# Kernel optimization log

Measured on AMD Instinct MI355X. Metric: run time of the kernel, lower is better.

The kernel has to match this reference:

```python
import jax, jax.numpy as jnp
import numpy as np

HIDDEN = 256
GROUPS = 4
GDIM = HIDDEN // GROUPS  # 64


def setup_inputs() -> dict:
    key = jax.random.key(0)
    k1, k2, k3, k4 = jax.random.split(key, 4)
    B, N, P = 8, 300, 32
    x = jax.random.normal(k1, (B, N, P, HIDDEN), dtype=jnp.float32)
    query_content = jax.random.normal(k2, (B, N, HIDDEN), dtype=jnp.float32)
    out_dim = GDIM * GDIM * GROUPS
    # nn.Linear default init: U(-1/sqrt(fan_in), 1/sqrt(fan_in))
    bound = 1.0 / np.sqrt(HIDDEN)
    W_gen = jax.random.uniform(k3, (HIDDEN, out_dim), dtype=jnp.float32, minval=-bound, maxval=bound)
    b_gen = jax.random.uniform(k4, (out_dim,), dtype=jnp.float32, minval=-bound, maxval=bound)
    gamma = jnp.ones((HIDDEN,), dtype=jnp.float32)
    beta = jnp.zeros((HIDDEN,), dtype=jnp.float32)
    return {"x": x, "query_content": query_content, "W_gen": W_gen, "b_gen": b_gen, "gamma": gamma, "beta": beta}


def _layer_norm(h, gamma, beta, eps=1e-5):
    mu = jnp.mean(h, axis=-1, keepdims=True)
    var = jnp.var(h, axis=-1, keepdims=True)
    return (h - mu) * jax.lax.rsqrt(var + eps) * gamma + beta


def reference(x, query_content, W_gen, b_gen, gamma, beta):
    B, N, P, C = x.shape
    # dynamic per-query weights: [B,N,G,gd,gd]
    w = (query_content @ W_gen + b_gen).reshape(B, N, GROUPS, GDIM, GDIM)
    xg = x.reshape(B, N, P, GROUPS, GDIM)
    # mixed[...,p,g,e] = sum_d xg[...,p,g,d] * w[...,g,e,d]  (matmul with W^T)
    mixed = jnp.einsum('bnpgd,bnged->bnpge', xg, w).reshape(B, N, P, C)
    return jax.nn.relu(_layer_norm(mixed, gamma, beta))
```

## Files before the change

kernel.cpp:

```cpp
#include <hip/hip_runtime.h>
#include <hip/hip_bf16.h>

typedef __attribute__((ext_vector_type(4))) float floatx4;
typedef __attribute__((ext_vector_type(8))) short short8;

#define HIDDEN 256
#define NOUT 16384

static __device__ __forceinline__ short bf16bits(float x) {
    __hip_bfloat16 h = __float2bfloat16(x);
    return __builtin_bit_cast(short, h);
}

#define GLDS16(gsrc, ldst) \
    __builtin_amdgcn_global_load_lds((const __attribute__((address_space(1))) void*)(gsrc), \
                                     (__attribute__((address_space(3))) void*)(ldst), 16, 0, 0)

static __device__ __forceinline__ int permc(int c) {
    const int g = c >> 12, e = (c >> 6) & 63, d = c & 63;
    const int nt = e >> 4, lq = e & 15, ks = (d >> 5) & 1, quad = (d >> 3) & 3, j = d & 7;
    return ((((g << 2) | nt) << 1 | ks) << 9) | (((quad << 4) | lq) << 3) | j;
}
static __device__ __forceinline__ int invperm(int p) {
    const int blk = p >> 9, g = blk >> 3, nt = (blk >> 1) & 3, ks = blk & 1;
    const int r = (p >> 3) & 63, quad = r >> 4, lq = r & 15, j = p & 7;
    return g * 4096 + (nt * 16 + lq) * 64 + ks * 32 + quad * 8 + j;
}

__global__ __launch_bounds__(256) void kPrep(
    const float* __restrict__ Wg, short* __restrict__ WgTp,
    const float* __restrict__ qc, short* __restrict__ qcb, int n4)
{
    __shared__ short t[64 * 68];
    const int tid = threadIdx.x;

    if (blockIdx.x < 1024) {
        const int n0 = (blockIdx.x & 255) * 64, k0 = (blockIdx.x >> 8) * 64;
        const int r  = tid >> 4;
        const int c4 = tid & 15;
        #pragma unroll
        for (int i = 0; i < 4; ++i) {
            const int kl = r + i * 16;
            float4 f = *reinterpret_cast<const float4*>(Wg + (size_t)(k0 + kl) * NOUT + n0 + c4 * 4);
            short4 v;
            v.x = bf16bits(f.x); v.y = bf16bits(f.y); v.z = bf16bits(f.z); v.w = bf16bits(f.w);
            *reinterpret_cast<short4*>(&t[kl * 68 + c4 * 4]) = v;
        }
        __syncthreads();
        #pragma unroll
        for (int h = 0; h < 2; ++h) {
            const int id = tid + h * 256;
            const int nl = id >> 3, kc = id & 7;
            short8 v;
            #pragma unroll
            for (int j = 0; j < 8; ++j) v[j] = t[(kc * 8 + j) * 68 + nl];
            const int prow = permc(n0 + nl);
            *reinterpret_cast<short8*>(WgTp + (size_t)prow * HIDDEN + k0 + kc * 8) = v;
        }
    } else {
        const int i = (blockIdx.x - 1024) * 256 + tid;
        if (i < n4) {
            float4 f = reinterpret_cast<const float4*>(qc)[i];
            short4 v;
            v.x = bf16bits(f.x); v.y = bf16bits(f.y); v.z = bf16bits(f.z); v.w = bf16bits(f.w);
            reinterpret_cast<short4*>(qcb)[i] = v;
        }
    }
}

__global__ __launch_bounds__(256) void kA5(
    const short* __restrict__ qcb, const short* __restrict__ WgTp,
    const float* __restrict__ bg, short* __restrict__ wdyn, int M)
{
    __shared__ short As[128 * 64];
    __shared__ short Bs[128 * 64];

    const int tid  = threadIdx.x;
    const int wave = tid >> 6, lane = tid & 63;
    const int lq   = lane & 15, quad = lane >> 4;
    const int wm   = wave >> 1, wn = wave & 1;
    const int m0   = blockIdx.x * 128;
    const int n0   = blockIdx.y * 128;

    const short* aSrc[4]; const short* bSrc[4];
    short* aDst[4]; short* bDst[4];
    #pragma unroll
    for (int t = 0; t < 4; ++t) {
        const int chunk = t * 256 + wave * 64 + lane;
        const int row = chunk >> 3, kc = chunk & 7;
        const int kcs = kc ^ (row & 7);
        int rA = m0 + row; if (rA >= M) rA = M - 1;
        aSrc[t] = qcb  + (size_t)rA * HIDDEN + kcs * 8;
        bSrc[t] = WgTp + (size_t)(n0 + row) * HIDDEN + kcs * 8;
        aDst[t] = &As[(t * 256 + wave * 64) * 8];
        bDst[t] = &Bs[(t * 256 + wave * 64) * 8];
    }

    int aOff[2][4], bOff[2][4];
    #pragma unroll
    for (int ks = 0; ks < 2; ++ks)
        #pragma unroll
        for (int i = 0; i < 4; ++i) {
            const int ra = wm * 64 + i * 16 + lq;
            aOff[ks][i] = ra * 64 + (((ks * 4 + quad) ^ (ra & 7)) * 8);
            const int rb = wn * 64 + i * 16 + lq;
            bOff[ks][i] = rb * 64 + (((ks * 4 + quad) ^ (rb & 7)) * 8);
        }

    floatx4 acc[4][4];
    #pragma unroll
    for (int i = 0; i < 4; ++i)
        #pragma unroll
        for (int j = 0; j < 4; ++j) acc[i][j] = (floatx4){0.f, 0.f, 0.f, 0.f};

    for (int it = 0; it < 4; ++it) {
        #pragma unroll
        for (int t = 0; t < 4; ++t) {
            GLDS16(aSrc[t], aDst[t]);
            GLDS16(bSrc[t], bDst[t]);
            aSrc[t] += 64; bSrc[t] += 64;
        }
        __syncthreads();

        #pragma unroll
        for (int ks = 0; ks < 2; ++ks) {
            short8 a[4], b[4];
            #pragma unroll
            for (int i = 0; i < 4; ++i) a[i] = *reinterpret_cast<const short8*>(&As[aOff[ks][i]]);
            #pragma unroll
            for (int j = 0; j < 4; ++j) b[j] = *reinterpret_cast<const short8*>(&Bs[bOff[ks][j]]);
            #pragma unroll
            for (int i = 0; i < 4; ++i)
                #pragma unroll
                for (int j = 0; j < 4; ++j)
                    acc[i][j] = __builtin_amdgcn_mfma_f32_16x16x32_bf16(a[i], b[j], acc[i][j], 0, 0, 0);
        }
        __syncthreads();
    }

    float bv[4];
    #pragma unroll
    for (int j = 0; j < 4; ++j) bv[j] = bg[invperm(n0 + wn * 64 + j * 16 + lq)];

    short* Cs = As;
    #pragma unroll
    for (int half = 0; half < 2; ++half) {
        if (half) __syncthreads();
        if (wm == half) {
            #pragma unroll
            for (int j = 0; j < 4; ++j)
                #pragma unroll
                for (int i = 0; i < 4; ++i)
                    #pragma unroll
                    for (int r = 0; r < 4; ++r)
                        Cs[(i * 16 + quad * 4 + r) * 128 + wn * 64 + j * 16 + lq] =
                            bf16bits(acc[i][j][r] + bv[j]);
        }
        __syncthreads();
        #pragma unroll
        for (int t = 0; t < 4; ++t) {
            const int id = t * 256 + tid;
            const int mr = id >> 4, ch = id & 15;
            const int grow = m0 + half * 64 + mr;
            if (grow < M)
                *reinterpret_cast<short8*>(&wdyn[(size_t)grow * NOUT + n0 + ch * 8]) =
                    *reinterpret_cast<const short8*>(&Cs[mr * 128 + ch * 8]);
        }
    }
}

__global__ __launch_bounds__(256) void kB6(
    const float* __restrict__ x, const short* __restrict__ wdyn,
    const float* __restrict__ gamma, const float* __restrict__ beta,
    float* __restrict__ out)
{
    __shared__ float ots[16 * 256];
    __shared__ float red[2][2][16][2];

    const int tid  = threadIdx.x;
    const int bnq  = blockIdx.x;
    const int wave = tid >> 6, lane = tid & 63;
    const int lq   = lane & 15, quad = lane >> 4;
    const int mtile = wave & 1, gp = wave >> 1;

    const float* xr = x + (size_t)bnq * (32 * HIDDEN) + (mtile * 16 + lq) * HIDDEN;
    const short* wr = wdyn + (size_t)bnq * NOUT + lane * 8;

    floatx4 xf[2][2][2];
    #pragma unroll
    for (int gi = 0; gi < 2; ++gi) {
        const int g = gp * 2 + gi;
        #pragma unroll
        for (int ks = 0; ks < 2; ++ks) {
            const floatx4* s = reinterpret_cast<const floatx4*>(xr + g * 64 + ks * 32 + quad * 8);
            xf[gi][ks][0] = __builtin_nontemporal_load(s);
            xf[gi][ks][1] = __builtin_nontemporal_load(s + 1);
        }
    }
    short8 afr[2][2];
    #pragma unroll
    for (int gi = 0; gi < 2; ++gi)
        #pragma unroll
        for (int ks = 0; ks < 2; ++ks) {
            const floatx4 f0 = xf[gi][ks][0];
            const floatx4 f1 = xf[gi][ks][1];
            short8 v;
            v[0]=bf16bits(f0[0]); v[1]=bf16bits(f0[1]); v[2]=bf16bits(f0[2]); v[3]=bf16bits(f0[3]);
            v[4]=bf16bits(f1[0]); v[5]=bf16bits(f1[1]); v[6]=bf16bits(f1[2]); v[7]=bf16bits(f1[3]);
            afr[gi][ks] = v;
        }

    floatx4 acc[2][4];
    #pragma unroll
    for (int gi = 0; gi < 2; ++gi)
        #pragma unroll
        for (int nt = 0; nt < 4; ++nt) acc[gi][nt] = (floatx4){0.f, 0.f, 0.f, 0.f};

    #pragma unroll
    for (int gi = 0; gi < 2; ++gi) {
        const int g = gp * 2 + gi;
        #pragma unroll
        for (int ks = 0; ks < 2; ++ks) {
            short8 b[4];
            #pragma unroll
            for (int nt = 0; nt < 4; ++nt)
                b[nt] = *reinterpret_cast<const short8*>(
                    wr + (((((g << 2) | nt) << 1) | ks) << 9));
            #pragma unroll
            for (int nt = 0; nt < 4; ++nt)
                acc[gi][nt] = __builtin_amdgcn_mfma_f32_16x16x32_bf16(
                    b[nt], afr[gi][ks], acc[gi][nt], 0, 0, 0);
        }
    }

    float s = 0.f, ss = 0.f;
    #pragma unroll
    for (int gi = 0; gi < 2; ++gi)
        #pragma unroll
        for (int nt = 0; nt < 4; ++nt)
            #pragma unroll
            for (int r = 0; r < 4; ++r) {
                const float v = acc[gi][nt][r];
                s += v; ss += v * v;
            }
    s  += __shfl_xor(s, 16);  ss += __shfl_xor(ss, 16);
    s  += __shfl_xor(s, 32);  ss += __shfl_xor(ss, 32);

    if (quad == 0) { red[mtile][gp][lq][0] = s; red[mtile][gp][lq][1] = ss; }
    __syncthreads();

    const float S  = s  + red[mtile][gp ^ 1][lq][0];
    const float SS = ss + red[mtile][gp ^ 1][lq][1];
    const float mu = S * (1.f / 256.f);
    float var = SS * (1.f / 256.f) - mu * mu;
    var = fmaxf(var, 0.f);
    const float rs = rsqrtf(var + 1e-5f);

    #pragma unroll
    for (int gi = 0; gi < 2; ++gi) {
        const int g = gp * 2 + gi;
        #pragma unroll
        for (int nt = 0; nt < 4; ++nt) {
            const int c0 = g * 64 + nt * 16 + quad * 4;
            const floatx4 gm = *reinterpret_cast<const floatx4*>(gamma + c0);
            const floatx4 bt = *reinterpret_cast<const floatx4*>(beta + c0);
            #pragma unroll
            for (int r = 0; r < 4; ++r)
                acc[gi][nt][r] = fmaxf((acc[gi][nt][r] - mu) * rs * gm[r] + bt[r], 0.f);
        }
    }

    floatx4* ots4 = reinterpret_cast<floatx4*>(ots);
    floatx4* obase = reinterpret_cast<floatx4*>(out + (size_t)bnq * (32 * HIDDEN));
    #pragma unroll
    for (int h = 0; h < 2; ++h) {
        if (h) __syncthreads();
        if (mtile == h) {
            #pragma unroll
            for (int gi = 0; gi < 2; ++gi) {
                const int g = gp * 2 + gi;
                #pragma unroll
                for (int nt = 0; nt < 4; ++nt) {
                    const int c4 = g * 16 + nt * 4 + quad;
                    ots4[(lq * 64 + c4) ^ (lq & 7)] = acc[gi][nt];
                }
            }
        }
        __syncthreads();
        #pragma unroll
        for (int t = 0; t < 4; ++t) {
            const int sl = t * 256 + tid;
            const int pl = sl >> 6;
            const floatx4 v = ots4[sl ^ (pl & 7)];
            __builtin_nontemporal_store(v, obase + h * 1024 + sl);
        }
    }
}

extern "C" void kernel_launch(void* const* d_in, const int* in_sizes, int n_in,
                              void* d_out, int out_size, void* d_ws, size_t ws_size,
                              hipStream_t stream)
{
    const float* x     = (const float*)d_in[0];
    const float* qc    = (const float*)d_in[1];
    const float* Wg    = (const float*)d_in[2];
    const float* bg    = (const float*)d_in[3];
    const float* gamma = (const float*)d_in[4];
    const float* beta  = (const float*)d_in[5];
    float* out = (float*)d_out;

    const int M = in_sizes[1] / HIDDEN;

    char* ws = (char*)d_ws;
    short* wdyn = (short*)ws;
    short* WgTp = (short*)(ws + (size_t)M * NOUT * 2);
    short* qcb  = (short*)(ws + (size_t)M * NOUT * 2 + (size_t)NOUT * HIDDEN * 2);

    const int n4 = (M * HIDDEN) / 4;
    const int prepBlocks = 1024 + (n4 + 255) / 256;
    kPrep<<<prepBlocks, 256, 0, stream>>>(Wg, WgTp, qc, qcb, n4);

    kA5<<<dim3((M + 127) / 128, NOUT / 128), 256, 0, stream>>>(qcb, WgTp, bg, wdyn, M);

    kB6<<<M, 256, 0, stream>>>(x, wdyn, gamma, beta, out);
}
```

Before: 217.3 us.

## Pre-swizzle GEMM operands into MFMA fragment order and load directly to registers

The prep kernel now writes the bf16 weight and query matrices in a fragment-tiled layout that matches the 16x16x32 MFMA operand layout. The GEMM then reads each operand straight from global memory into registers with double-buffered prefetch, dropping the LDS staging and barriers. Work-group indices are also remapped so each XCD handles a contiguous band of N tiles, which should improve L2 reuse of the weight panel. In exchange, operand tiles are re-read from global/L2 by each wave without LDS sharing, and M rows past the last 16-row tile are clamped to tile 0, which assumes M is a multiple of 16.

```diff
diff --git a/kernel.cpp b/kernel.cpp
--- a/kernel.cpp
+++ b/kernel.cpp
@@ -11,10 +11,6 @@
     __hip_bfloat16 h = __float2bfloat16(x);
     return __builtin_bit_cast(short, h);
 }
-
-#define GLDS16(gsrc, ldst) \
-    __builtin_amdgcn_global_load_lds((const __attribute__((address_space(1))) void*)(gsrc), \
-                                     (__attribute__((address_space(3))) void*)(ldst), 16, 0, 0)
 
 static __device__ __forceinline__ int permc(int c) {
     const int g = c >> 12, e = (c >> 6) & 63, d = c & 63;
@@ -28,8 +24,8 @@
 }
 
 __global__ __launch_bounds__(256) void kPrep(
-    const float* __restrict__ Wg, short* __restrict__ WgTp,
-    const float* __restrict__ qc, short* __restrict__ qcb, int n4)
+    const float* __restrict__ Wg, short* __restrict__ WgF,
+    const float* __restrict__ qc, short* __restrict__ qcF, int n4)
 {
     __shared__ short t[64 * 68];
     const int tid = threadIdx.x;
@@ -55,7 +51,8 @@
             #pragma unroll
             for (int j = 0; j < 8; ++j) v[j] = t[(kc * 8 + j) * 68 + nl];
             const int prow = permc(n0 + nl);
-            *reinterpret_cast<short8*>(WgTp + (size_t)prow * HIDDEN + k0 + kc * 8) = v;
+            const int q = (k0 >> 3) + kc;
+            *reinterpret_cast<short8*>(WgF + (size_t)(prow >> 4) * 4096 + q * 128 + (prow & 15) * 8) = v;
         }
     } else {
         const int i = (blockIdx.x - 1024) * 256 + tid;
@@ -63,49 +60,44 @@
             float4 f = reinterpret_cast<const float4*>(qc)[i];
             short4 v;
             v.x = bf16bits(f.x); v.y = bf16bits(f.y); v.z = bf16bits(f.z); v.w = bf16bits(f.w);
-            reinterpret_cast<short4*>(qcb)[i] = v;
-        }
-    }
-}
-
-__global__ __launch_bounds__(256) void kA5(
-    const short* __restrict__ qcb, const short* __restrict__ WgTp,
+            const int m = i >> 6, k4 = i & 63;
+            const int off = (m >> 4) * 4096 + (k4 >> 1) * 128 + (m & 15) * 8 + (k4 & 1) * 4;
+            *reinterpret_cast<short4*>(qcF + off) = v;
+        }
+    }
+}
+
+__global__ __launch_bounds__(256) void kA6(
+    const short* __restrict__ qcF, const short* __restrict__ WgF,
     const float* __restrict__ bg, short* __restrict__ wdyn, int M)
 {
-    __shared__ short As[128 * 64];
-    __shared__ short Bs[128 * 64];
+    __shared__ short Cs[64 * 128];
 
     const int tid  = threadIdx.x;
     const int wave = tid >> 6, lane = tid & 63;
     const int lq   = lane & 15, quad = lane >> 4;
     const int wm   = wave >> 1, wn = wave & 1;
-    const int m0   = blockIdx.x * 128;
-    const int n0   = blockIdx.y * 128;
-
-    const short* aSrc[4]; const short* bSrc[4];
-    short* aDst[4]; short* bDst[4];
-    #pragma unroll
-    for (int t = 0; t < 4; ++t) {
-        const int chunk = t * 256 + wave * 64 + lane;
-        const int row = chunk >> 3, kc = chunk & 7;
-        const int kcs = kc ^ (row & 7);
-        int rA = m0 + row; if (rA >= M) rA = M - 1;
-        aSrc[t] = qcb  + (size_t)rA * HIDDEN + kcs * 8;
-        bSrc[t] = WgTp + (size_t)(n0 + row) * HIDDEN + kcs * 8;
-        aDst[t] = &As[(t * 256 + wave * 64) * 8];
-        bDst[t] = &Bs[(t * 256 + wave * 64) * 8];
-    }
-
-    int aOff[2][4], bOff[2][4];
-    #pragma unroll
-    for (int ks = 0; ks < 2; ++ks)
-        #pragma unroll
-        for (int i = 0; i < 4; ++i) {
-            const int ra = wm * 64 + i * 16 + lq;
-            aOff[ks][i] = ra * 64 + (((ks * 4 + quad) ^ (ra & 7)) * 8);
-            const int rb = wn * 64 + i * 16 + lq;
-            bOff[ks][i] = rb * 64 + (((ks * 4 + quad) ^ (rb & 7)) * 8);
-        }
+
+    const int wgid = blockIdx.x;
+    const int xcd  = wgid & 7;
+    const int c    = wgid >> 3;
+    const int nMB  = gridDim.x >> 7;
+    const int pl   = c / nMB;
+    const int mi   = c - pl * nMB;
+    const int m0   = mi * 128;
+    const int n0   = (xcd * 16 + pl) * 128;
+
+    const int mtMax = M >> 4;
+    const int mT0 = (m0 >> 4) + wm * 4;
+    const int nT0 = (n0 >> 4) + wn * 4;
+
+    const short* aB[4]; const short* bB[4];
+    #pragma unroll
+    for (int i = 0; i < 4; ++i) {
+        int mT = mT0 + i; if (mT >= mtMax) mT = 0;
+        aB[i] = qcF + (size_t)mT * 4096 + lane * 8;
+        bB[i] = WgF + (size_t)(nT0 + i) * 4096 + lane * 8;
+    }
 
     floatx4 acc[4][4];
     #pragma unroll
@@ -113,36 +105,33 @@
         #pragma unroll
         for (int j = 0; j < 4; ++j) acc[i][j] = (floatx4){0.f, 0.f, 0.f, 0.f};
 
-    for (int it = 0; it < 4; ++it) {
-        #pragma unroll
-        for (int t = 0; t < 4; ++t) {
-            GLDS16(aSrc[t], aDst[t]);
-            GLDS16(bSrc[t], bDst[t]);
-            aSrc[t] += 64; bSrc[t] += 64;
-        }
-        __syncthreads();
-
-        #pragma unroll
-        for (int ks = 0; ks < 2; ++ks) {
-            short8 a[4], b[4];
-            #pragma unroll
-            for (int i = 0; i < 4; ++i) a[i] = *reinterpret_cast<const short8*>(&As[aOff[ks][i]]);
-            #pragma unroll
-            for (int j = 0; j < 4; ++j) b[j] = *reinterpret_cast<const short8*>(&Bs[bOff[ks][j]]);
-            #pragma unroll
-            for (int i = 0; i < 4; ++i)
-                #pragma unroll
-                for (int j = 0; j < 4; ++j)
-                    acc[i][j] = __builtin_amdgcn_mfma_f32_16x16x32_bf16(a[i], b[j], acc[i][j], 0, 0, 0);
-        }
-        __syncthreads();
+    short8 A[2][4], B[2][4];
+    #pragma unroll
+    for (int i = 0; i < 4; ++i) {
+        A[0][i] = *reinterpret_cast<const short8*>(aB[i]);
+        B[0][i] = *reinterpret_cast<const short8*>(bB[i]);
+    }
+    #pragma unroll
+    for (int step = 0; step < 8; ++step) {
+        const int cur = step & 1, nxt = cur ^ 1;
+        if (step < 7) {
+            #pragma unroll
+            for (int i = 0; i < 4; ++i) {
+                A[nxt][i] = *reinterpret_cast<const short8*>(aB[i] + (step + 1) * 512);
+                B[nxt][i] = *reinterpret_cast<const short8*>(bB[i] + (step + 1) * 512);
+            }
+        }
+        #pragma unroll
+        for (int i = 0; i < 4; ++i)
+            #pragma unroll
+            for (int j = 0; j < 4; ++j)
+                acc[i][j] = __builtin_amdgcn_mfma_f32_16x16x32_bf16(A[cur][i], B[cur][j], acc[i][j], 0, 0, 0);
     }
 
     float bv[4];
     #pragma unroll
     for (int j = 0; j < 4; ++j) bv[j] = bg[invperm(n0 + wn * 64 + j * 16 + lq)];
 
-    short* Cs = As;
     #pragma unroll
     for (int half = 0; half < 2; ++half) {
         if (half) __syncthreads();
@@ -313,14 +302,15 @@
 
     char* ws = (char*)d_ws;
     short* wdyn = (short*)ws;
-    short* WgTp = (short*)(ws + (size_t)M * NOUT * 2);
-    short* qcb  = (short*)(ws + (size_t)M * NOUT * 2 + (size_t)NOUT * HIDDEN * 2);
+    short* WgF  = (short*)(ws + (size_t)M * NOUT * 2);
+    short* qcF  = (short*)(ws + (size_t)M * NOUT * 2 + (size_t)NOUT * HIDDEN * 2);
 
     const int n4 = (M * HIDDEN) / 4;
     const int prepBlocks = 1024 + (n4 + 255) / 256;
-    kPrep<<<prepBlocks, 256, 0, stream>>>(Wg, WgTp, qc, qcb, n4);
-
-    kA5<<<dim3((M + 127) / 128, NOUT / 128), 256, 0, stream>>>(qcb, WgTp, bg, wdyn, M);
+    kPrep<<<prepBlocks, 256, 0, stream>>>(Wg, WgF, qc, qcF, n4);
+
+    const int nMB = (M + 127) / 128;
+    kA6<<<nMB * 128, 256, 0, stream>>>(qcF, WgF, bg, wdyn, M);
 
     kB6<<<M, 256, 0, stream>>>(x, wdyn, gamma, beta, out);
 }
```

After: 217.2 us. Within noise of the previous version (-0.1%).
